# Kernel optimization log

Measured on AMD Instinct MI355X. Metric: run time of the kernel, lower is better.

The kernel has to match this reference:

```python
import jax, jax.numpy as jnp
import numpy as np


def setup_inputs() -> dict:
    key = jax.random.key(0)
    kp, ka = jax.random.split(key)
    N, A = 100000, 1024
    # points: xyz over a 100m x 100m plot, z in [0, 30] (tree heights)
    u = jax.random.uniform(kp, (N, 3), dtype=jnp.float32)
    points = u * jnp.array([100.0, 100.0, 30.0], dtype=jnp.float32)
    # anchors: [cx, cy, cz, w, l, h]
    ua = jax.random.uniform(ka, (A, 6), dtype=jnp.float32)
    cx = ua[:, 0] * 100.0
    cy = ua[:, 1] * 100.0
    cz = jnp.zeros((A,), jnp.float32)
    w = 2.0 + ua[:, 3] * 6.0
    l = 2.0 + ua[:, 4] * 6.0
    h = 10.0 + ua[:, 5] * 20.0
    anchors = jnp.stack([cx, cy, cz, w, l, h], axis=1)
    return {"points": points, "anchors": anchors, "n": 512}


def _roi_point_pool(points, anchors, n):
    """Vectorised per-anchor point-in-box pooling (TreeRCNN._subsample_points_batch).

    Returns padded [A, n, 3] anchor-local points (x,y translated by anchor
    center, z untouched) and per-anchor clamped counts. Slots >= count are 0.
    Selection of the first-n in-box points is deterministic in point order
    (the torch code uses a random tie-break key; determinism chosen for a
    reproducible correctness baseline — same gather/scatter structure).
    """
    A = anchors.shape[0]
    N = points.shape[0]
    px, py, pz = points[:, 0], points[:, 1], points[:, 2]
    cx, cy = anchors[:, 0:1], anchors[:, 1:2]
    w, l, h = anchors[:, 3:4], anchors[:, 4:5], anchors[:, 5:6]
    # [A, N] box-membership mask (the O(A*N) traffic-bound hot loop)
    mask = ((px >= cx - w * 0.5) & (px <= cx + w * 0.5)
            & (py >= cy - l * 0.5) & (py <= cy + l * 0.5)
            & (pz >= 0.0) & (pz <= h))
    # per-anchor local slot index for each in-box point
    local = jnp.cumsum(mask.astype(jnp.int32), axis=1) - 1          # [A, N]
    valid = mask & (local < n)
    counts = valid.sum(axis=1)                                      # [A]
    # scatter point ids (+1 so 0 marks empty) into flat padded slots;
    # invalid hits go to a dump slot A*n
    flat = jnp.where(valid,
                     jnp.arange(A, dtype=jnp.int32)[:, None] * n + local,
                     A * n)
    vals = (jnp.arange(N, dtype=jnp.int32)[None, :] + 1) * valid
    pid = jnp.zeros(A * n + 1, jnp.int32).at[flat.reshape(-1)].add(vals.reshape(-1))
    pid = pid[: A * n].reshape(A, n)                                # [A, n]
    points_ext = jnp.concatenate([jnp.zeros((1, 3), points.dtype), points], axis=0)
    padded = points_ext[pid]                                        # [A, n, 3]
    # translate x,y to anchor-local coords on filled slots only
    centers = jnp.concatenate([anchors[:, :2], jnp.zeros((A, 1), anchors.dtype)], axis=1)
    padded = jnp.where(pid[..., None] > 0, padded - centers[:, None, :], 0.0)
    return padded, counts


def reference(points, anchors, n):
    return _roi_point_pool(points, anchors, n)
```

## Files before the change

### kernel.cpp

```cpp
#include <hip/hip_runtime.h>


#define NB     128
#define NBB    (NB * NB)
#define CAPB   32
#define NWRD   3584
#define WPT    7
#define MAXBIN 160

__global__ __launch_bounds__(256) void scatter_kernel(
    const float* __restrict__ pts, int* __restrict__ bincnt,
    float4* __restrict__ bucket, int N)
{
    const int t4 = blockIdx.x * 256 + threadIdx.x;
    const int i0 = t4 * 4;
    if (i0 >= N) return;
    const float s = NB / 100.0f;

    if (i0 + 4 <= N) {
        const float4* pb = (const float4*)(pts + 3 * i0);
        const float4 q0 = pb[0], q1 = pb[1], q2 = pb[2];
        const float px[4] = {q0.x, q0.w, q1.z, q2.y};
        const float py[4] = {q0.y, q1.x, q1.w, q2.z};
        const float pz[4] = {q0.z, q1.y, q2.x, q2.w};
        #pragma unroll
        for (int u = 0; u < 4; ++u) {
            const int bx = min(NB - 1, (int)(px[u] * s));
            const int by = min(NB - 1, (int)(py[u] * s));
            const int bin = by * NB + bx;
            const int slot = atomicAdd(&bincnt[bin], 1);
            if (slot < CAPB)
                bucket[bin * CAPB + slot] =
                    make_float4(px[u], py[u], pz[u], __int_as_float(i0 + u));
        }
    } else {
        for (int i = i0; i < N; ++i) {
            const float px = pts[3 * i + 0], py = pts[3 * i + 1], pz = pts[3 * i + 2];
            const int bx = min(NB - 1, (int)(px * s));
            const int by = min(NB - 1, (int)(py * s));
            const int bin = by * NB + bx;
            const int slot = atomicAdd(&bincnt[bin], 1);
            if (slot < CAPB)
                bucket[bin * CAPB + slot] = make_float4(px, py, pz, __int_as_float(i));
        }
    }
}

__global__ __launch_bounds__(512) void anchor_kernel(
    const float* __restrict__ pts, const float* __restrict__ anc,
    const int* __restrict__ bincnt, const float4* __restrict__ bucket,
    float* __restrict__ out_pts, float* __restrict__ out_cnt, int n)
{
    const int a    = blockIdx.x;
    const int tid  = threadIdx.x;
    const int lane = tid & 63;
    const int wave = tid >> 6;

    const float cx = anc[a * 6 + 0], cy = anc[a * 6 + 1];
    const float w  = anc[a * 6 + 3], l  = anc[a * 6 + 4], h = anc[a * 6 + 5];
    const float xl = cx - w * 0.5f, xh = cx + w * 0.5f;
    const float yl = cy - l * 0.5f, yh = cy + l * 0.5f;

    __shared__ unsigned int s_mask[NWRD];
    __shared__ int s_bcnt[MAXBIN];
    __shared__ int s_wsum[8], s_wpre[9];

    #pragma unroll
    for (int u = 0; u < WPT; ++u) s_mask[tid + u * 512] = 0u;

    const float sc = NB / 100.0f;
    const int bx0 = max(0, (int)floorf(xl * sc));
    const int bx1 = min(NB - 1, (int)floorf(xh * sc));
    const int by0 = max(0, (int)floorf(yl * sc));
    const int by1 = min(NB - 1, (int)floorf(yh * sc));
    const int nbx = bx1 - bx0 + 1;
    const int nby = by1 - by0 + 1;
    const int nbins = (nbx > 0 && nby > 0) ? nbx * nby : 0;

    for (int t = tid; t < nbins; t += 512) {
        const int by = by0 + t / nbx, bx = bx0 + t % nbx;
        s_bcnt[t] = min(bincnt[by * NB + bx], CAPB);
    }
    __syncthreads();

    const int tot = nbins << 5;
    for (int t = tid; t < tot; t += 512) {
        const int slot = t & (CAPB - 1);
        const int b    = t >> 5;
        if (slot < s_bcnt[b]) {
            const int bin  = (by0 + b / nbx) * NB + bx0 + b % nbx;
            const float4 p = bucket[bin * CAPB + slot];
            if (p.x >= xl && p.x <= xh && p.y >= yl && p.y <= yh &&
                p.z >= 0.0f && p.z <= h) {
                const int idx = __float_as_int(p.w);
                atomicOr(&s_mask[idx >> 5], 1u << (idx & 31));
            }
        }
    }
    __syncthreads();

    const int wbase = tid * WPT;
    int s = 0;
    unsigned int mw[WPT];
    #pragma unroll
    for (int u = 0; u < WPT; ++u) {
        mw[u] = s_mask[wbase + u];
        s += __popc(mw[u]);
    }
    int incl = s;
    #pragma unroll
    for (int d = 1; d < 64; d <<= 1) {
        const int t = __shfl_up(incl, d);
        if (lane >= d) incl += t;
    }
    if (lane == 63) s_wsum[wave] = incl;
    __syncthreads();
    if (tid == 0) {
        int run = 0;
        #pragma unroll
        for (int v = 0; v < 8; ++v) { const int t = s_wsum[v]; s_wpre[v] = run; run += t; }
        s_wpre[8] = run;
    }
    __syncthreads();
    const int total = s_wpre[8];
    const int count = total < n ? total : n;
    int slot = s_wpre[wave] + incl - s;

    float* const outa = out_pts + (size_t)a * n * 3;
    #pragma unroll
    for (int u = 0; u < WPT; ++u) {
        unsigned int wm = mw[u];
        while (wm) {
            const int b = __ffs(wm) - 1;
            wm &= wm - 1u;
            if (slot < n) {
                const int i = (wbase + u) * 32 + b;
                outa[3 * slot + 0] = pts[3 * i + 0] - cx;
                outa[3 * slot + 1] = pts[3 * i + 1] - cy;
                outa[3 * slot + 2] = pts[3 * i + 2];
            }
            ++slot;
        }
    }

    for (int t = count * 3 + tid; t < n * 3; t += 512) outa[t] = 0.f;
    if (tid == 0) out_cnt[a] = (float)count;
}

__global__ __launch_bounds__(256) void roi_pool_kernel(
    const float* __restrict__ pts, const float* __restrict__ anc,
    float* __restrict__ out_pts, float* __restrict__ out_cnt, int N, int n)
{
    const int a = blockIdx.x;
    const float cx = anc[a * 6 + 0], cy = anc[a * 6 + 1];
    const float w  = anc[a * 6 + 3], l  = anc[a * 6 + 4], h = anc[a * 6 + 5];
    const float xmin = cx - 0.5f * w, xmax = cx + 0.5f * w;
    const float ymin = cy - 0.5f * l, ymax = cy + 0.5f * l;
    const int tid = threadIdx.x, wave = tid >> 6, lane = tid & 63;
    __shared__ int s_tot[4];
    int base = 0;
    float* const outa = out_pts + (size_t)a * n * 3;
    for (int start = 0; start < N; start += 256) {
        const int i = start + tid;
        bool m = false;
        float px = 0.f, py = 0.f, pz = 0.f;
        if (i < N) {
            px = pts[3 * i]; py = pts[3 * i + 1]; pz = pts[3 * i + 2];
            m = (px >= xmin) & (px <= xmax) & (py >= ymin) & (py <= ymax) &
                (pz >= 0.0f) & (pz <= h);
        }
        const unsigned long long ball = __ballot(m);
        const int lanePfx = __popcll(ball & ((1ull << lane) - 1ull));
        if (lane == 0) s_tot[wave] = __popcll(ball);
        __syncthreads();
        const int t0 = s_tot[0], t1 = s_tot[1], t2 = s_tot[2], t3 = s_tot[3];
        int offs = base;
        if (wave > 0) offs += t0;
        if (wave > 1) offs += t1;
        if (wave > 2) offs += t2;
        const int slot = offs + lanePfx;
        if (m && slot < n) {
            float* o = outa + (size_t)slot * 3;
            o[0] = px - cx; o[1] = py - cy; o[2] = pz;
        }
        base += t0 + t1 + t2 + t3;
        __syncthreads();
        if (base >= n) break;
    }
    const int count = base < n ? base : n;
    if (tid == 0) out_cnt[a] = (float)count;
    for (int s = count + tid; s < n; s += 256) {
        float* o = outa + (size_t)s * 3;
        o[0] = 0.f; o[1] = 0.f; o[2] = 0.f;
    }
}

extern "C" void kernel_launch(void* const* d_in, const int* in_sizes, int n_in,
                              void* d_out, int out_size, void* d_ws, size_t ws_size,
                              hipStream_t stream) {
    const float* pts = (const float*)d_in[0];
    const float* anc = (const float*)d_in[1];
    const int N = in_sizes[0] / 3;
    const int A = in_sizes[1] / 6;
    const int n = (out_size / A - 1) / 3;

    float* out_pts = (float*)d_out;
    float* out_cnt = (float*)d_out + (size_t)A * n * 3;

    const size_t bucket_bytes = (size_t)NBB * CAPB * sizeof(float4);
    const size_t cnt_bytes    = (size_t)NBB * sizeof(int);
    const size_t total_ws     = bucket_bytes + cnt_bytes;

    if (ws_size < total_ws || N > NWRD * 32) {
        roi_pool_kernel<<<dim3(A), dim3(256), 0, stream>>>(pts, anc, out_pts, out_cnt, N, n);
        return;
    }

    float4* bucket = (float4*)d_ws;
    int* bincnt    = (int*)((char*)d_ws + bucket_bytes);

    hipMemsetAsync(bincnt, 0, cnt_bytes, stream);

    const int pb4 = (N + 1023) / 1024;
    scatter_kernel<<<dim3(pb4), dim3(256), 0, stream>>>(pts, bincnt, bucket, N);
    anchor_kernel<<<dim3(A), dim3(512), 0, stream>>>(pts, anc, bincnt, bucket,
                                                     out_pts, out_cnt, n);
}
```

Baseline: 80.50 us.

## Fuse memset, binning scatter and per-anchor pooling into one cooperative kernel

Replaces the memset plus two launches with a single cooperative kernel of 1024 blocks of 256 threads. Grid-wide syncs separate the bin-count clear, the point scatter into spatial buckets and the per-anchor mask/prefix/compaction stage. The goal is to remove launch and inter-kernel gaps. In exchange each anchor block now has 256 threads instead of 512, so each thread scans twice as many mask words, and the kernel pays for two grid barriers. The fallback scatter path also drops its 4-points-per-thread vectorised load.

```diff
diff --git a/kernel.cpp b/kernel.cpp
--- a/kernel.cpp
+++ b/kernel.cpp
@@ -1,49 +1,151 @@
 #include <hip/hip_runtime.h>
+#include <hip/hip_cooperative_groups.h>
+
+namespace cg = cooperative_groups;
 
 
 #define NB     128
 #define NBB    (NB * NB)
 #define CAPB   32
 #define NWRD   3584
-#define WPT    7
+#define WPT    14
 #define MAXBIN 160
+
+__global__ __launch_bounds__(256) void fused_kernel(
+    const float* __restrict__ pts, const float* __restrict__ anc,
+    int* __restrict__ bincnt, float4* __restrict__ bucket,
+    float* __restrict__ out_pts, float* __restrict__ out_cnt,
+    int N, int n, int A)
+{
+    const int tid  = threadIdx.x;
+    const int gt   = blockIdx.x * 256 + tid;
+    const int lane = tid & 63;
+    const int wave = tid >> 6;
+
+    if (gt < NBB) bincnt[gt] = 0;
+    cg::this_grid().sync();
+
+    if (gt < N) {
+        const float px = pts[3 * gt + 0], py = pts[3 * gt + 1], pz = pts[3 * gt + 2];
+        const float s = NB / 100.0f;
+        const int bx = min(NB - 1, (int)(px * s));
+        const int by = min(NB - 1, (int)(py * s));
+        const int bin = by * NB + bx;
+        const int slot = atomicAdd(&bincnt[bin], 1);
+        if (slot < CAPB)
+            bucket[bin * CAPB + slot] = make_float4(px, py, pz, __int_as_float(gt));
+    }
+    cg::this_grid().sync();
+
+    const int a = blockIdx.x;
+    if (a >= A) return;
+
+    const float cx = anc[a * 6 + 0], cy = anc[a * 6 + 1];
+    const float w  = anc[a * 6 + 3], l  = anc[a * 6 + 4], h = anc[a * 6 + 5];
+    const float xl = cx - w * 0.5f, xh = cx + w * 0.5f;
+    const float yl = cy - l * 0.5f, yh = cy + l * 0.5f;
+
+    __shared__ unsigned int s_mask[NWRD];
+    __shared__ int s_bcnt[MAXBIN];
+    __shared__ int s_wsum[4], s_wpre[5];
+
+    #pragma unroll
+    for (int u = 0; u < WPT; ++u) s_mask[tid + u * 256] = 0u;
+
+    const float sc = NB / 100.0f;
+    const int bx0 = max(0, (int)floorf(xl * sc));
+    const int bx1 = min(NB - 1, (int)floorf(xh * sc));
+    const int by0 = max(0, (int)floorf(yl * sc));
+    const int by1 = min(NB - 1, (int)floorf(yh * sc));
+    const int nbx = bx1 - bx0 + 1;
+    const int nby = by1 - by0 + 1;
+    const int nbins = (nbx > 0 && nby > 0) ? nbx * nby : 0;
+
+    for (int t = tid; t < nbins; t += 256) {
+        const int by = by0 + t / nbx, bx = bx0 + t % nbx;
+        s_bcnt[t] = min(bincnt[by * NB + bx], CAPB);
+    }
+    __syncthreads();
+
+    const int tot = nbins << 5;
+    for (int t = tid; t < tot; t += 256) {
+        const int slot = t & (CAPB - 1);
+        const int b    = t >> 5;
+        if (slot < s_bcnt[b]) {
+            const int bin  = (by0 + b / nbx) * NB + bx0 + b % nbx;
+            const float4 p = bucket[bin * CAPB + slot];
+            if (p.x >= xl && p.x <= xh && p.y >= yl && p.y <= yh &&
+                p.z >= 0.0f && p.z <= h) {
+                const int idx = __float_as_int(p.w);
+                atomicOr(&s_mask[idx >> 5], 1u << (idx & 31));
+            }
+        }
+    }
+    __syncthreads();
+
+    const int wbase = tid * WPT;
+    int s = 0;
+    unsigned int mw[WPT];
+    #pragma unroll
+    for (int u = 0; u < WPT; ++u) {
+        mw[u] = s_mask[wbase + u];
+        s += __popc(mw[u]);
+    }
+    int incl = s;
+    #pragma unroll
+    for (int d = 1; d < 64; d <<= 1) {
+        const int t = __shfl_up(incl, d);
+        if (lane >= d) incl += t;
+    }
+    if (lane == 63) s_wsum[wave] = incl;
+    __syncthreads();
+    if (tid == 0) {
+        int run = 0;
+        #pragma unroll
+        for (int v = 0; v < 4; ++v) { const int t = s_wsum[v]; s_wpre[v] = run; run += t; }
+        s_wpre[4] = run;
+    }
+    __syncthreads();
+    const int total2 = s_wpre[4];
+    const int count  = total2 < n ? total2 : n;
+    int slot = s_wpre[wave] + incl - s;
+
+    float* const outa = out_pts + (size_t)a * n * 3;
+    #pragma unroll
+    for (int u = 0; u < WPT; ++u) {
+        unsigned int wm = mw[u];
+        while (wm) {
+            const int b = __ffs(wm) - 1;
+            wm &= wm - 1u;
+            if (slot < n) {
+                const int i = (wbase + u) * 32 + b;
+                outa[3 * slot + 0] = pts[3 * i + 0] - cx;
+                outa[3 * slot + 1] = pts[3 * i + 1] - cy;
+                outa[3 * slot + 2] = pts[3 * i + 2];
+            }
+            ++slot;
+        }
+    }
+
+    for (int t = count * 3 + tid; t < n * 3; t += 256) outa[t] = 0.f;
+    if (tid == 0) out_cnt[a] = (float)count;
+}
+
 
 __global__ __launch_bounds__(256) void scatter_kernel(
     const float* __restrict__ pts, int* __restrict__ bincnt,
     float4* __restrict__ bucket, int N)
 {
-    const int t4 = blockIdx.x * 256 + threadIdx.x;
-    const int i0 = t4 * 4;
-    if (i0 >= N) return;
+    const int i = blockIdx.x * 256 + threadIdx.x;
+    if (i >= N) return;
+    const float px = pts[3 * i + 0], py = pts[3 * i + 1], pz = pts[3 * i + 2];
     const float s = NB / 100.0f;
-
-    if (i0 + 4 <= N) {
-        const float4* pb = (const float4*)(pts + 3 * i0);
-        const float4 q0 = pb[0], q1 = pb[1], q2 = pb[2];
-        const float px[4] = {q0.x, q0.w, q1.z, q2.y};
-        const float py[4] = {q0.y, q1.x, q1.w, q2.z};
-        const float pz[4] = {q0.z, q1.y, q2.x, q2.w};
-        #pragma unroll
-        for (int u = 0; u < 4; ++u) {
-            const int bx = min(NB - 1, (int)(px[u] * s));
-            const int by = min(NB - 1, (int)(py[u] * s));
-            const int bin = by * NB + bx;
-            const int slot = atomicAdd(&bincnt[bin], 1);
-            if (slot < CAPB)
-                bucket[bin * CAPB + slot] =
-                    make_float4(px[u], py[u], pz[u], __int_as_float(i0 + u));
-        }
-    } else {
-        for (int i = i0; i < N; ++i) {
-            const float px = pts[3 * i + 0], py = pts[3 * i + 1], pz = pts[3 * i + 2];
-            const int bx = min(NB - 1, (int)(px * s));
-            const int by = min(NB - 1, (int)(py * s));
-            const int bin = by * NB + bx;
-            const int slot = atomicAdd(&bincnt[bin], 1);
-            if (slot < CAPB)
-                bucket[bin * CAPB + slot] = make_float4(px, py, pz, __int_as_float(i));
-        }
-    }
+    const int bx = min(NB - 1, (int)(px * s));
+    const int by = min(NB - 1, (int)(py * s));
+    const int bin = by * NB + bx;
+    const int slot = atomicAdd(&bincnt[bin], 1);
+    if (slot < CAPB)
+        bucket[bin * CAPB + slot] = make_float4(px, py, pz, __int_as_float(i));
 }
 
 __global__ __launch_bounds__(512) void anchor_kernel(
@@ -66,7 +168,7 @@
     __shared__ int s_wsum[8], s_wpre[9];
 
     #pragma unroll
-    for (int u = 0; u < WPT; ++u) s_mask[tid + u * 512] = 0u;
+    for (int u = 0; u < 7; ++u) s_mask[tid + u * 512] = 0u;
 
     const float sc = NB / 100.0f;
     const int bx0 = max(0, (int)floorf(xl * sc));
@@ -99,11 +201,11 @@
     }
     __syncthreads();
 
-    const int wbase = tid * WPT;
+    const int wbase = tid * 7;
     int s = 0;
-    unsigned int mw[WPT];
-    #pragma unroll
-    for (int u = 0; u < WPT; ++u) {
+    unsigned int mw[7];
+    #pragma unroll
+    for (int u = 0; u < 7; ++u) {
         mw[u] = s_mask[wbase + u];
         s += __popc(mw[u]);
     }
@@ -128,7 +230,7 @@
 
     float* const outa = out_pts + (size_t)a * n * 3;
     #pragma unroll
-    for (int u = 0; u < WPT; ++u) {
+    for (int u = 0; u < 7; ++u) {
         unsigned int wm = mw[u];
         while (wm) {
             const int b = __ffs(wm) - 1;
@@ -142,7 +244,6 @@
             ++slot;
         }
     }
-
     for (int t = count * 3 + tid; t < n * 3; t += 512) outa[t] = 0.f;
     if (tid == 0) out_cnt[a] = (float)count;
 }
@@ -200,9 +301,9 @@
                               hipStream_t stream) {
     const float* pts = (const float*)d_in[0];
     const float* anc = (const float*)d_in[1];
-    const int N = in_sizes[0] / 3;
-    const int A = in_sizes[1] / 6;
-    const int n = (out_size / A - 1) / 3;
+    int N = in_sizes[0] / 3;
+    int A = in_sizes[1] / 6;
+    int n = (out_size / A - 1) / 3;
 
     float* out_pts = (float*)d_out;
     float* out_cnt = (float*)d_out + (size_t)A * n * 3;
@@ -219,10 +320,20 @@
     float4* bucket = (float4*)d_ws;
     int* bincnt    = (int*)((char*)d_ws + bucket_bytes);
 
-    hipMemsetAsync(bincnt, 0, cnt_bytes, stream);
-
-    const int pb4 = (N + 1023) / 1024;
-    scatter_kernel<<<dim3(pb4), dim3(256), 0, stream>>>(pts, bincnt, bucket, N);
-    anchor_kernel<<<dim3(A), dim3(512), 0, stream>>>(pts, anc, bincnt, bucket,
-                                                     out_pts, out_cnt, n);
-}
+    hipError_t cerr = hipErrorUnknown;
+    if (A <= 1024 && N <= 1024 * 256 && NBB <= 1024 * 256) {
+        void* args[] = {
+            (void*)&pts, (void*)&anc, (void*)&bincnt, (void*)&bucket,
+            (void*)&out_pts, (void*)&out_cnt, (void*)&N, (void*)&n, (void*)&A
+        };
+        cerr = hipLaunchCooperativeKernel((void*)fused_kernel, dim3(1024),
+                                          dim3(256), args, 0, stream);
+    }
+    if (cerr != hipSuccess) {
+        hipMemsetAsync(bincnt, 0, cnt_bytes, stream);
+        scatter_kernel<<<dim3((N + 255) / 256), dim3(256), 0, stream>>>(
+            pts, bincnt, bucket, N);
+        anchor_kernel<<<dim3(A), dim3(512), 0, stream>>>(
+            pts, anc, bincnt, bucket, out_pts, out_cnt, n);
+    }
+}
```

Result: slower. 249.7 us (+210.2%).
